# Kernel optimization log

Hardware: AMD Instinct MI355X
Metric: run time of the kernel (lower is better)

The kernel has to match this reference:

```python
import jax, jax.numpy as jnp
import numpy as np

B, N, T, DM, H, M = 32, 207, 24, 64, 8, 32
E = 2 * DM  # true input feature dim (2*dmodel per the reshape in the source)


def setup_inputs() -> dict:
    rng = jax.random.key(0)
    ks = jax.random.split(rng, 10)
    s = 0.05  # scale params to keep activations numerically sane
    query = jax.random.normal(ks[0], (B, N, T, E), jnp.float32)
    key = jax.random.normal(ks[1], (B, N, T, E), jnp.float32)
    value = jax.random.normal(ks[2], (B, N, T, E), jnp.float32)
    # causal temporal mask, broadcast over batch/node/head; True = masked out
    atten_mask = jnp.broadcast_to(jnp.triu(jnp.ones((T, T), bool), 1), (B, N, 1, T, T))
    qp1 = jax.random.normal(ks[3], (N * DM, M), jnp.float32) * s
    qp2 = jax.random.normal(ks[4], (M, 4 * DM), jnp.float32) * s
    kp1 = jax.random.normal(ks[5], (N * DM, M), jnp.float32) * s
    kp2 = jax.random.normal(ks[6], (M, 4 * DM), jnp.float32) * s
    vp1 = jax.random.normal(ks[7], (N * DM, M), jnp.float32) * s
    vp2 = jax.random.normal(ks[8], (M, 4 * DM), jnp.float32) * s
    out_W = jax.random.normal(ks[9], (E, DM), jnp.float32) * s
    out_b = jnp.zeros((DM,), jnp.float32)
    return dict(query=query, key=key, value=value, atten_mask=atten_mask,
                qp1=qp1, qp2=qp2, kp1=kp1, kp2=kp2, vp1=vp1, vp2=vp2,
                out_W=out_W, out_b=out_b, num_heads=H)


def reference(query, key, value, atten_mask, qp1, qp2, kp1, kp2, vp1, vp2, out_W, out_b, num_heads):
    b, n, t, e = query.shape

    def proj(x, p1, p2):
        # low-rank factored per-node projection: (N*dmodel, M) @ (M, 4*dmodel) -> (N, E, E)
        P = (p1 @ p2).reshape(n, e, e)
        y = jnp.einsum('bnti,nik->bntk', x, P)
        return jax.nn.relu(y).reshape(b, n, t, num_heads, -1)

    q = proj(query, qp1, qp2)   # (B,N,T,H,d)
    k = proj(key, kp1, kp2)
    v = proj(value, vp1, vp2)

    scale = 1.0 / np.sqrt(q.shape[-1]).astype(np.float32)
    scores = jnp.einsum('bnthe,bnshe->bnhts', q, k)          # (B,N,H,T,S)
    scores = jnp.where(atten_mask, -jnp.inf, scores)          # masked_fill before scaling
    attn = jax.nn.softmax(scale * scores, axis=-1)            # dropout disabled (eval)
    out = jnp.einsum('bnhts,bnshd->bnthd', attn, v).reshape(b, n, t, -1)
    out = jax.nn.relu(out @ out_W + out_b)                    # (B,N,T,dmodel)
    return out, attn
```

## Files before the change

### kernel.cpp

```cpp
#include <hip/hip_runtime.h>
#include <hip/hip_bf16.h>

#define Bn 32
#define Nn 207
#define Tt 24
#define Ee 128
#define Hh 8
#define Dm 64
#define Mm 32
#define NBN (Bn * Nn)
#define PT ((size_t)Nn * 16384)

typedef __attribute__((ext_vector_type(8))) short bf16x8;
typedef __attribute__((ext_vector_type(4))) float f32x4;

__device__ __forceinline__ unsigned swz256(unsigned a) { return a ^ (((a >> 8) & 7u) << 4); }
__device__ __forceinline__ unsigned cvtpk(float lo, float hi) {
  unsigned r;
  asm("v_cvt_pk_bf16_f32 %0, %1, %2" : "=v"(r) : "v"(lo), "v"(hi));
  return r;
}
__device__ __forceinline__ unsigned short f2bs(float f) {
  return (unsigned short)cvtpk(f, f);
}

__global__ __launch_bounds__(256) void build_P_frag3(
    const float* __restrict__ qp1, const float* __restrict__ qp2,
    const float* __restrict__ kp1, const float* __restrict__ kp2,
    const float* __restrict__ vp1, const float* __restrict__ vp2,
    unsigned short* __restrict__ Pt) {
  const int tau = blockIdx.y;
  const float* p1 = (tau == 0) ? qp1 : (tau == 1) ? kp1 : vp1;
  const float* p2 = (tau == 0) ? qp2 : (tau == 1) ? kp2 : vp2;
  unsigned short* dst = Pt + (size_t)tau * PT;
  const int bid = blockIdx.x;
  const int n = bid >> 3;
  const int r8 = bid & 7;
  const int ks = r8 >> 1;
  const int chunk = ((r8 & 1) << 1) + (threadIdx.x >> 7);
  const int col = threadIdx.x & 127;
  const int base_i = ks * 32 + chunk * 8;
  const float* p1r = p1 + (size_t)(n * 64 + (base_i >> 1)) * Mm;
  const float* p2a = p2 + col;
  const float* p2b = p2 + 128 + col;
  float acc[8] = {};
#pragma unroll
  for (int m = 0; m < Mm; ++m) {
    float a = p2a[m * 256], b = p2b[m * 256];
#pragma unroll
    for (int jj = 0; jj < 4; ++jj) {
      float pv = p1r[jj * Mm + m];
      acc[2 * jj]     = fmaf(pv, a, acc[2 * jj]);
      acc[2 * jj + 1] = fmaf(pv, b, acc[2 * jj + 1]);
    }
  }
  const int nt = col >> 4;
  const int lane = (chunk << 4) | (col & 15);
  union { unsigned u[4]; uint4 v; } w;
#pragma unroll
  for (int jj = 0; jj < 4; ++jj) w.u[jj] = cvtpk(acc[2 * jj], acc[2 * jj + 1]);
  *(uint4*)(dst + (size_t)(((n * 8 + nt) * 4 + ks) * 64 + lane) * 8) = w.v;
}

__global__ __launch_bounds__(256) void build_W_frag(const float* __restrict__ W,
                                                    unsigned short* __restrict__ Wt) {
  for (int idx = threadIdx.x; idx < 1024; idx += 256) {
    int lane = idx & 63, ks = (idx >> 6) & 3, nt = idx >> 8;
    union { unsigned u[4]; uint4 v; } w;
#pragma unroll
    for (int jj = 0; jj < 4; ++jj) {
      float a = W[(size_t)(ks * 32 + (lane >> 4) * 8 + 2 * jj) * 64 + nt * 16 + (lane & 15)];
      float b = W[(size_t)(ks * 32 + (lane >> 4) * 8 + 2 * jj + 1) * 64 + nt * 16 + (lane & 15)];
      w.u[jj] = cvtpk(a, b);
    }
    *(uint4*)(Wt + (size_t)idx * 8) = w.v;
  }
}

struct P8 { unsigned u[8]; };

__global__ __launch_bounds__(256, 6) void fused_attn(
    const float* __restrict__ Qin, const float* __restrict__ Kin,
    const float* __restrict__ Vin,
    const unsigned short* __restrict__ Ptq, const unsigned short* __restrict__ Ptk,
    const unsigned short* __restrict__ Ptv, const unsigned short* __restrict__ Wt,
    const float* __restrict__ bias,
    float* __restrict__ out, float* __restrict__ attn) {
  __shared__ __align__(16) char smem[24576];
  const int tid = threadIdx.x;
  const int lane = tid & 63;
  const int wv = tid >> 6;
  const int c = lane & 15;
  const int g = lane >> 4;
  const f32x4 zf = {0.f, 0.f, 0.f, 0.f};
  const bf16x8 zb = {0, 0, 0, 0, 0, 0, 0, 0};

  int bx = blockIdx.x;
  bx = (bx & 7) * 828 + (bx >> 3);
  const int n = bx >> 5;
  const int b = bx & 31;
  const size_t xbase = (size_t)(b * Nn + n) * (Tt * Ee);

  {
    const float* src[3] = {Qin + xbase, Kin + xbase, Vin + xbase};
#pragma unroll
    for (int w = 0; w < 3; ++w)
#pragma unroll
      for (int it = 0; it < 3; ++it) {
        int e4 = tid + 256 * it;
        float4 xv = *(const float4*)(src[w] + (size_t)e4 * 4);
        unsigned a = swz256((unsigned)((e4 >> 5) * 256 + (e4 & 31) * 8));
        uint2 pk;
        pk.x = cvtpk(xv.x, xv.y);
        pk.y = cvtpk(xv.z, xv.w);
        *(uint2*)(smem + w * 6144 + a) = pk;
      }
  }
  __syncthreads();

  P8 pq, pk_, pv_;
  {
#pragma unroll
    for (int w = 0; w < 3; ++w) {
      const unsigned short* Pf = (w == 0) ? Ptq : (w == 1) ? Ptk : Ptv;
      const char* xs = smem + w * 6144;
      f32x4 acc[2][2] = {{zf, zf}, {zf, zf}};
#pragma unroll
      for (int ks = 0; ks < 4; ++ks) {
        bf16x8 Bf[2], Af[2];
#pragma unroll
        for (int ntl = 0; ntl < 2; ++ntl)
          Bf[ntl] = *(const bf16x8*)(Pf + (size_t)(((n * 8 + (wv * 2 + ntl)) * 4 + ks) * 64 + lane) * 8);
#pragma unroll
        for (int mt = 0; mt < 2; ++mt) {
          int row = mt * 16 + c; row = row < 24 ? row : 23;
          Af[mt] = *(const bf16x8*)(xs + swz256((unsigned)(row * 256 + ks * 64 + g * 16)));
        }
        __builtin_amdgcn_s_setprio(1);
#pragma unroll
        for (int mt = 0; mt < 2; ++mt)
#pragma unroll
          for (int ntl = 0; ntl < 2; ++ntl)
            acc[mt][ntl] = __builtin_amdgcn_mfma_f32_16x16x32_bf16(Af[mt], Bf[ntl], acc[mt][ntl], 0, 0, 0);
        __builtin_amdgcn_s_setprio(0);
      }
      const float ps = (w == 0) ? 0.25f : 1.0f;
      P8 r;
#pragma unroll
      for (int mt = 0; mt < 2; ++mt)
#pragma unroll
        for (int ntl = 0; ntl < 2; ++ntl)
#pragma unroll
          for (int half = 0; half < 2; ++half) {
            float a = fmaxf(acc[mt][ntl][half * 2], 0.f) * ps;
            float bb = fmaxf(acc[mt][ntl][half * 2 + 1], 0.f) * ps;
            r.u[(mt * 2 + ntl) * 2 + half] = cvtpk(a, bb);
          }
      if (w == 0) pq = r; else if (w == 1) pk_ = r; else pv_ = r;
    }
  }
  __syncthreads();

  char* arena = smem + wv * 4608;

#pragma unroll
  for (int mt = 0; mt < 2; ++mt)
#pragma unroll
    for (int ntl = 0; ntl < 2; ++ntl)
#pragma unroll
      for (int half = 0; half < 2; ++half) {
        unsigned uq = pq.u[(mt * 2 + ntl) * 2 + half];
        unsigned uk = pk_.u[(mt * 2 + ntl) * 2 + half];
        unsigned uv = pv_.u[(mt * 2 + ntl) * 2 + half];
#pragma unroll
        for (int rr = 0; rr < 2; ++rr) {
          int row = mt * 16 + g * 4 + half * 2 + rr;
          if (row < 24) {
            unsigned short vq = (unsigned short)(rr ? (uq >> 16) : uq);
            unsigned short vk = (unsigned short)(rr ? (uk >> 16) : uk);
            unsigned short vvv = (unsigned short)(rr ? (uv >> 16) : uv);
            unsigned adqk = (unsigned)(row * 64) +
                            (((unsigned)(ntl * 32 + c * 2)) ^ (((unsigned)row & 3u) << 4));
            *(unsigned short*)(arena + adqk) = vq;
            *(unsigned short*)(arena + 1536 + adqk) = vk;
            *(unsigned short*)(arena + 3072 + (ntl * 16 + c) * 48 + row * 2) = vvv;
          }
        }
      }

  bf16x8 Aq[2][2], Bk[2][2];
#pragma unroll
  for (int hh = 0; hh < 2; ++hh)
#pragma unroll
    for (int mt = 0; mt < 2; ++mt) {
      int row = mt * 16 + c; row = row < 24 ? row : 23;
      unsigned ad = (unsigned)(row * 64) +
                    (((unsigned)(hh * 32 + g * 16)) ^ (((unsigned)row & 3u) << 4));
      Aq[hh][mt] = zb;
      Bk[hh][mt] = zb;
      if (g < 2) {
        Aq[hh][mt] = *(const bf16x8*)(arena + ad);
        Bk[hh][mt] = *(const bf16x8*)(arena + 1536 + ad);
      }
    }

  unsigned pk0[8];
#pragma unroll
  for (int hh = 0; hh < 2; ++hh) {
    f32x4 sc[2][2];
    __builtin_amdgcn_s_setprio(1);
#pragma unroll
    for (int mt = 0; mt < 2; ++mt)
#pragma unroll
      for (int st = 0; st < 2; ++st)
        sc[mt][st] = __builtin_amdgcn_mfma_f32_16x16x32_bf16(Aq[hh][mt], Bk[hh][st], zf, 0, 0, 0);
    __builtin_amdgcn_s_setprio(0);
#pragma unroll
    for (int mt = 0; mt < 2; ++mt)
#pragma unroll
      for (int r = 0; r < 4; ++r) {
        int t = mt * 16 + g * 4 + r;
        float e0 = (c <= t)      ? __expf(sc[mt][0][r]) : 0.f;
        float e1 = (16 + c <= t) ? __expf(sc[mt][1][r]) : 0.f;
        float s2 = e0 + e1;
        s2 += __shfl_xor(s2, 1);
        s2 += __shfl_xor(s2, 2);
        s2 += __shfl_xor(s2, 4);
        s2 += __shfl_xor(s2, 8);
        float inv = 1.0f / s2;
        float p0 = e0 * inv, p1 = e1 * inv;
        if (hh == 0) {
          pk0[mt * 4 + r] = cvtpk(p0, p1);
        } else {
          if (t < 24) {
            *(unsigned short*)(arena + 1152 + t * 48 + c * 2) = f2bs(p0);
            if (c < 8) *(unsigned short*)(arena + 1152 + t * 48 + (16 + c) * 2) = f2bs(p1);
          }
        }
      }
  }
#pragma unroll
  for (int mt = 0; mt < 2; ++mt)
#pragma unroll
    for (int r = 0; r < 4; ++r) {
      int t = mt * 16 + g * 4 + r;
      if (t < 24) {
        unsigned u = pk0[mt * 4 + r];
        *(unsigned short*)(arena + t * 48 + c * 2) = (unsigned short)u;
        if (c < 8) *(unsigned short*)(arena + t * 48 + (16 + c) * 2) = (unsigned short)(u >> 16);
      }
    }

  {
    bf16x8 Ap[2][2], Bv[2];
#pragma unroll
    for (int hh = 0; hh < 2; ++hh) {
      Bv[hh] = zb;
      if (g < 3) Bv[hh] = *(const bf16x8*)(arena + 3072 + (hh * 16 + c) * 48 + g * 16);
#pragma unroll
      for (int mt = 0; mt < 2; ++mt) {
        int row = mt * 16 + c; row = row < 24 ? row : 23;
        Ap[hh][mt] = zb;
        if (g < 3) Ap[hh][mt] = *(const bf16x8*)(arena + hh * 1152 + row * 48 + g * 16);
      }
    }
    const size_t abase = (size_t)(b * Nn + n) * (Hh * Tt * Tt);
#pragma unroll
    for (int i = 0; i < 5; ++i) {
      int idx = lane + 64 * i;
      if (idx < 288) {
        int hh = idx / 144;
        int rem = idx - hh * 144;
        int t = rem / 6;
        int s4g = rem - t * 6;
        uint2 pr = *(const uint2*)(arena + hh * 1152 + t * 48 + s4g * 8);
        float4 o;
        o.x = __uint_as_float((pr.x & 0xFFFFu) << 16);
        o.y = __uint_as_float(pr.x & 0xFFFF0000u);
        o.z = __uint_as_float((pr.y & 0xFFFFu) << 16);
        o.w = __uint_as_float(pr.y & 0xFFFF0000u);
        *(float4*)(attn + abase + (size_t)(wv * 2 + hh) * 576 + t * 24 + s4g * 4) = o;
      }
    }
    f32x4 pv[2][2];
    __builtin_amdgcn_s_setprio(1);
#pragma unroll
    for (int hh = 0; hh < 2; ++hh)
#pragma unroll
      for (int mt = 0; mt < 2; ++mt)
        pv[hh][mt] = __builtin_amdgcn_mfma_f32_16x16x32_bf16(Ap[hh][mt], Bv[hh], zf, 0, 0, 0);
    __builtin_amdgcn_s_setprio(0);
#pragma unroll
    for (int hh = 0; hh < 2; ++hh) {
      int h = wv * 2 + hh;
#pragma unroll
      for (int mt = 0; mt < 2; ++mt)
#pragma unroll
        for (int r = 0; r < 4; ++r) {
          int t = mt * 16 + g * 4 + r;
          if (t < 24)
            *(unsigned short*)(smem + 18432 + swz256((unsigned)(t * 256 + (h * 16 + c) * 2))) =
                f2bs(pv[hh][mt][r]);
        }
    }
  }

  bf16x8 Bw[4];
#pragma unroll
  for (int ks = 0; ks < 4; ++ks)
    Bw[ks] = *(const bf16x8*)(Wt + (size_t)((wv * 4 + ks) * 64 + lane) * 8);
  __syncthreads();

  {
    f32x4 acc2[2] = {zf, zf};
#pragma unroll
    for (int ks = 0; ks < 4; ++ks) {
      bf16x8 Af[2];
#pragma unroll
      for (int mt = 0; mt < 2; ++mt) {
        int row = mt * 16 + c; row = row < 24 ? row : 23;
        Af[mt] = *(const bf16x8*)(smem + 18432 + swz256((unsigned)(row * 256 + ks * 64 + g * 16)));
      }
      __builtin_amdgcn_s_setprio(1);
#pragma unroll
      for (int mt = 0; mt < 2; ++mt)
        acc2[mt] = __builtin_amdgcn_mfma_f32_16x16x32_bf16(Af[mt], Bw[ks], acc2[mt], 0, 0, 0);
      __builtin_amdgcn_s_setprio(0);
    }
    int j = wv * 16 + c;
    float bj = bias[j];
    const size_t obase = (size_t)(b * Nn + n) * (Tt * Dm);
#pragma unroll
    for (int mt = 0; mt < 2; ++mt)
#pragma unroll
      for (int r = 0; r < 4; ++r) {
        int t = mt * 16 + g * 4 + r;
        if (t < 24) out[obase + (size_t)t * Dm + j] = fmaxf(acc2[mt][r] + bj, 0.f);
      }
  }
}

extern "C" void kernel_launch(void* const* d_in, const int* in_sizes, int n_in,
                              void* d_out, int out_size, void* d_ws, size_t ws_size,
                              hipStream_t stream) {
  const float* query = (const float*)d_in[0];
  const float* key   = (const float*)d_in[1];
  const float* value = (const float*)d_in[2];
  const float* qp1 = (const float*)d_in[4];
  const float* qp2 = (const float*)d_in[5];
  const float* kp1 = (const float*)d_in[6];
  const float* kp2 = (const float*)d_in[7];
  const float* vp1 = (const float*)d_in[8];
  const float* vp2 = (const float*)d_in[9];
  const float* out_W = (const float*)d_in[10];
  const float* out_b = (const float*)d_in[11];

  unsigned short* Pt  = (unsigned short*)d_ws;
  unsigned short* Wtf = Pt + 3 * PT;

  float* out = (float*)d_out;
  float* attn = out + (size_t)NBN * Tt * Dm;

  build_P_frag3<<<dim3(Nn * 8, 3), 256, 0, stream>>>(qp1, qp2, kp1, kp2, vp1, vp2, Pt);
  build_W_frag<<<1, 256, 0, stream>>>(out_W, Wtf);
  fused_attn<<<NBN, 256, 0, stream>>>(query, key, value,
                                      Pt, Pt + PT, Pt + 2 * PT, Wtf,
                                      out_b, out, attn);
}
```

Measured before the change: 161.0 us.

## Defer softmax normalization via MFMA row-sum with ones vector; pack V stores

```diff
diff --git a/kernel.cpp b/kernel.cpp
--- a/kernel.cpp
+++ b/kernel.cpp
@@ -172,18 +172,19 @@
         unsigned uq = pq.u[(mt * 2 + ntl) * 2 + half];
         unsigned uk = pk_.u[(mt * 2 + ntl) * 2 + half];
         unsigned uv = pv_.u[(mt * 2 + ntl) * 2 + half];
+        int row0 = mt * 16 + g * 4 + half * 2;
+        if (row0 < 24)
+          *(unsigned*)(arena + 3072 + (ntl * 16 + c) * 48 + row0 * 2) = uv;
 #pragma unroll
         for (int rr = 0; rr < 2; ++rr) {
-          int row = mt * 16 + g * 4 + half * 2 + rr;
+          int row = row0 + rr;
           if (row < 24) {
             unsigned short vq = (unsigned short)(rr ? (uq >> 16) : uq);
             unsigned short vk = (unsigned short)(rr ? (uk >> 16) : uk);
-            unsigned short vvv = (unsigned short)(rr ? (uv >> 16) : uv);
             unsigned adqk = (unsigned)(row * 64) +
                             (((unsigned)(ntl * 32 + c * 2)) ^ (((unsigned)row & 3u) << 4));
             *(unsigned short*)(arena + adqk) = vq;
             *(unsigned short*)(arena + 1536 + adqk) = vk;
-            *(unsigned short*)(arena + 3072 + (ntl * 16 + c) * 48 + row * 2) = vvv;
           }
         }
       }
@@ -204,7 +205,6 @@
       }
     }
 
-  unsigned pk0[8];
 #pragma unroll
   for (int hh = 0; hh < 2; ++hh) {
     f32x4 sc[2][2];
@@ -222,37 +222,20 @@
         int t = mt * 16 + g * 4 + r;
         float e0 = (c <= t)      ? __expf(sc[mt][0][r]) : 0.f;
         float e1 = (16 + c <= t) ? __expf(sc[mt][1][r]) : 0.f;
-        float s2 = e0 + e1;
-        s2 += __shfl_xor(s2, 1);
-        s2 += __shfl_xor(s2, 2);
-        s2 += __shfl_xor(s2, 4);
-        s2 += __shfl_xor(s2, 8);
-        float inv = 1.0f / s2;
-        float p0 = e0 * inv, p1 = e1 * inv;
-        if (hh == 0) {
-          pk0[mt * 4 + r] = cvtpk(p0, p1);
-        } else {
-          if (t < 24) {
-            *(unsigned short*)(arena + 1152 + t * 48 + c * 2) = f2bs(p0);
-            if (c < 8) *(unsigned short*)(arena + 1152 + t * 48 + (16 + c) * 2) = f2bs(p1);
-          }
-        }
-      }
-  }
-#pragma unroll
-  for (int mt = 0; mt < 2; ++mt)
-#pragma unroll
-    for (int r = 0; r < 4; ++r) {
-      int t = mt * 16 + g * 4 + r;
-      if (t < 24) {
-        unsigned u = pk0[mt * 4 + r];
-        *(unsigned short*)(arena + t * 48 + c * 2) = (unsigned short)u;
-        if (c < 8) *(unsigned short*)(arena + t * 48 + (16 + c) * 2) = (unsigned short)(u >> 16);
-      }
-    }
+        if (t < 24) {
+          unsigned u = cvtpk(e0, e1);
+          *(unsigned short*)(arena + hh * 1152 + t * 48 + c * 2) = (unsigned short)u;
+          if (c < 8)
+            *(unsigned short*)(arena + hh * 1152 + t * 48 + (16 + c) * 2) = (unsigned short)(u >> 16);
+        }
+      }
+  }
 
   {
     bf16x8 Ap[2][2], Bv[2];
+    const short one_bf = (short)0x3F80;
+    bf16x8 onesf = {one_bf, one_bf, one_bf, one_bf, one_bf, one_bf, one_bf, one_bf};
+    if (g >= 3) onesf = zb;
 #pragma unroll
     for (int hh = 0; hh < 2; ++hh) {
       Bv[hh] = zb;
@@ -264,6 +247,37 @@
         if (g < 3) Ap[hh][mt] = *(const bf16x8*)(arena + hh * 1152 + row * 48 + g * 16);
       }
     }
+    f32x4 pv[2][2], su[2][2];
+    __builtin_amdgcn_s_setprio(1);
+#pragma unroll
+    for (int hh = 0; hh < 2; ++hh)
+#pragma unroll
+      for (int mt = 0; mt < 2; ++mt) {
+        su[hh][mt] = __builtin_amdgcn_mfma_f32_16x16x32_bf16(Ap[hh][mt], onesf, zf, 0, 0, 0);
+        pv[hh][mt] = __builtin_amdgcn_mfma_f32_16x16x32_bf16(Ap[hh][mt], Bv[hh], zf, 0, 0, 0);
+      }
+    __builtin_amdgcn_s_setprio(0);
+#pragma unroll
+    for (int hh = 0; hh < 2; ++hh)
+#pragma unroll
+      for (int mt = 0; mt < 2; ++mt) {
+        float iv[4];
+#pragma unroll
+        for (int r = 0; r < 4; ++r) {
+          iv[r] = __builtin_amdgcn_rcpf(su[hh][mt][r]);
+          pv[hh][mt][r] *= iv[r];
+        }
+        if (c == 0) {
+#pragma unroll
+          for (int rp = 0; rp < 4; rp += 2) {
+            int t0 = mt * 16 + g * 4 + rp;
+            if (t0 < 24) {
+              float2 st2 = {iv[rp], iv[rp + 1]};
+              *(float2*)(arena + 2304 + hh * 96 + t0 * 4) = st2;
+            }
+          }
+        }
+      }
     const size_t abase = (size_t)(b * Nn + n) * (Hh * Tt * Tt);
 #pragma unroll
     for (int i = 0; i < 5; ++i) {
@@ -274,22 +288,15 @@
         int t = rem / 6;
         int s4g = rem - t * 6;
         uint2 pr = *(const uint2*)(arena + hh * 1152 + t * 48 + s4g * 8);
+        float iv0 = *(const float*)(arena + 2304 + hh * 96 + t * 4);
         float4 o;
-        o.x = __uint_as_float((pr.x & 0xFFFFu) << 16);
-        o.y = __uint_as_float(pr.x & 0xFFFF0000u);
-        o.z = __uint_as_float((pr.y & 0xFFFFu) << 16);
-        o.w = __uint_as_float(pr.y & 0xFFFF0000u);
+        o.x = __uint_as_float((pr.x & 0xFFFFu) << 16) * iv0;
+        o.y = __uint_as_float(pr.x & 0xFFFF0000u) * iv0;
+        o.z = __uint_as_float((pr.y & 0xFFFFu) << 16) * iv0;
+        o.w = __uint_as_float(pr.y & 0xFFFF0000u) * iv0;
         *(float4*)(attn + abase + (size_t)(wv * 2 + hh) * 576 + t * 24 + s4g * 4) = o;
       }
     }
-    f32x4 pv[2][2];
-    __builtin_amdgcn_s_setprio(1);
-#pragma unroll
-    for (int hh = 0; hh < 2; ++hh)
-#pragma unroll
-      for (int mt = 0; mt < 2; ++mt)
-        pv[hh][mt] = __builtin_amdgcn_mfma_f32_16x16x32_bf16(Ap[hh][mt], Bv[hh], zf, 0, 0, 0);
-    __builtin_amdgcn_s_setprio(0);
 #pragma unroll
     for (int hh = 0; hh < 2; ++hh) {
       int h = wv * 2 + hh;
```

New measurement: 149.1 us (median of 2 runs). 1.08x faster.
